# Performance work log

Measured on AMD Instinct MI355X. Metric: run time of the kernel, lower is better.

## Reference

```python
import jax, jax.numpy as jnp
from jax import lax
import numpy as np

L_BANDS = 28
H = 1024
W = 1024


def setup_inputs() -> dict:
    key = jax.random.key(0)
    k1, k2 = jax.random.split(key)
    x_1lhw = jax.random.uniform(k1, (1, L_BANDS, H, W), dtype=jnp.float32)
    mask2d = jax.random.uniform(k2, (H, W), dtype=jnp.float32)
    phi_d_deg = jnp.ones((1,), dtype=jnp.float32)  # dispersion axis angle in degrees
    s_nom = 2.0 * jnp.arange(L_BANDS, dtype=jnp.float32)  # 2 px/band nominal dispersion
    return {"x_1lhw": x_1lhw, "mask2d": mask2d, "phi_d_deg": phi_d_deg, "s_nom": s_nom}


def _int_offsets(phi_d_deg, s_nom):
    # Mirrors torch: offsets come from .item() => detached constants.
    phi = float(np.asarray(phi_d_deg).reshape(())) * np.pi / 180.0
    s = np.asarray(s_nom, dtype=np.float64)
    dx = s * np.cos(phi)
    dy = s * np.sin(phi)
    dx = dx - dx.min()
    dy = dy - dy.min()
    return np.rint(dx).astype(np.int32), np.rint(dy).astype(np.int32)


def reference(x_1lhw, mask2d, phi_d_deg, s_nom):
    _, L, Hh, Ww = x_1lhw.shape
    dx_i, dy_i = _int_offsets(phi_d_deg, s_nom)
    Hp = Hh + int(dy_i.max())
    Wp = Ww + int(dx_i.max())
    bands = mask2d[None, :, :] * x_1lhw[0]  # [L, H, W] coded bands

    def step(y, inp):
        band, oy, ox = inp
        patch = lax.dynamic_slice(y, (oy, ox), (Hh, Ww)) + band
        return lax.dynamic_update_slice(y, patch, (oy, ox)), None

    y0 = jnp.zeros((Hp, Wp), dtype=x_1lhw.dtype)
    y, _ = lax.scan(step, y0, (bands, jnp.asarray(dy_i), jnp.asarray(dx_i)))
    return y[None]  # [1, Hp, Wp]
```

## Files before the change

kernel.cpp:

```cpp
#include <hip/hip_runtime.h>
#include <math.h>

#define NL 28
#define H 1024
#define W 1024
#define HW (H * W)
#define BROW 1152
#define GUARD 64
#define NWAVE 2
#define WBANDS 14
#define NBUF 3
#define WREG (NBUF * BROW)
#define NPASS 9

typedef float f2 __attribute__((ext_vector_type(2), aligned(4)));

typedef __attribute__((address_space(1))) const void GV;
typedef __attribute__((address_space(3))) void LV;
__device__ __forceinline__ void gl_lds16(const float* g, float* l) {
    __builtin_amdgcn_global_load_lds((GV*)g, (LV*)l, 16, 0, 0);
}

__global__ __launch_bounds__(128, 2)
void cassi_v12(const float* __restrict__ x, const float* __restrict__ mask,
               const float* __restrict__ phi_deg, const float* __restrict__ s_nom,
               float* __restrict__ out, int out_size)
{
    __shared__ float lds[NWAVE * WREG + 2 * BROW];

    const int tid = threadIdx.x;
    const int lane = tid & 63;
    const int wid = tid >> 6;

    float phi = phi_deg[0] * 0.017453292519943295f;
    float c = cosf(phi), sn = sinf(phi);
    float s = (lane < NL) ? s_nom[lane] : 0.f;
    float dxv = s * c, dyv = s * sn;
    float dxm = (lane < NL) ? dxv : 3.0e38f;
    float dym = (lane < NL) ? dyv : 3.0e38f;
    for (int d = 1; d < 64; d <<= 1) {
        dxm = fminf(dxm, __shfl_xor(dxm, d, 64));
        dym = fminf(dym, __shfl_xor(dym, d, 64));
    }
    int dxi = (lane < NL) ? (int)rintf(dxv - dxm) : 0;
    int dyi = (lane < NL) ? (int)rintf(dyv - dym) : 0;
    int dxmax = dxi, dymax = dyi;
    for (int d = 1; d < 64; d <<= 1) {
        dxmax = max(dxmax, __shfl_xor(dxmax, d, 64));
        dymax = max(dymax, __shfl_xor(dymax, d, 64));
    }
    const int Wp = W + dxmax;
    const int Hp = out_size / Wp;

    if (!(dymax <= 1 && dxmax <= GUARD)) {
        for (int i = blockIdx.x * 128 + tid; i < out_size; i += gridDim.x * 128) {
            int Yk = i / Wp, Xk = i - Yk * Wp;
            float a = 0.f;
            for (int l = 0; l < NL; ++l) {
                float sl = s_nom[l];
                int dx = (int)rintf(sl * c - dxm);
                int dy = (int)rintf(sl * sn - dym);
                int h = Yk - dy, w = Xk - dx;
                if ((unsigned)h < (unsigned)H && (unsigned)w < (unsigned)W) {
                    int p = h * W + w;
                    a = fmaf(mask[p], x[(size_t)l * HW + p], a);
                }
            }
            out[i] = a;
        }
        return;
    }

    const int Y = blockIdx.x;
    if (Y >= Hp) return;

    float* xw = &lds[wid * WREG];
    float* mb = &lds[NWAVE * WREG];

    int xo_[WBANDS], mo_[WBANDS], sr_[WBANDS];
#pragma unroll
    for (int j = 0; j < WBANDS; ++j) {
        int l = wid * WBANDS + j;
        int dxj = __shfl(dxi, l, 64);
        int dyj = __shfl(dyi, l, 64);
        xo_[j] = (j % NBUF) * BROW + GUARD - dxj;
        mo_[j] = dyj * BROW + GUARD - dxj;
        sr_[j] = min(max(Y - dyj, 0), H - 1);
    }

#pragma unroll
    for (int b = 0; b < NBUF; ++b) {
        xw[b * BROW + lane] = 0.f;
        xw[b * BROW + GUARD + 1024 + lane] = 0.f;
    }
    {
        int g = Y - wid;
        float* mrow = &mb[wid * BROW];
        if ((unsigned)g < (unsigned)H) {
            const float* src = mask + (size_t)g * W + lane * 4;
            gl_lds16(src,       mrow + GUARD);
            gl_lds16(src + 256, mrow + GUARD + 256);
            gl_lds16(src + 512, mrow + GUARD + 512);
            gl_lds16(src + 768, mrow + GUARD + 768);
            mrow[lane] = 0.f;
            mrow[GUARD + 1024 + lane] = 0.f;
        } else {
            for (int k = lane; k < BROW; k += 64) mrow[k] = 0.f;
        }
    }
#pragma unroll
    for (int j = 0; j < 2; ++j) {
        int l = wid * WBANDS + j;
        const float* src = x + (size_t)l * HW + (size_t)sr_[j] * W + lane * 4;
        float* dst = xw + j * BROW + GUARD;
        gl_lds16(src, dst);
        gl_lds16(src + 256, dst + 256);
        gl_lds16(src + 512, dst + 512);
        gl_lds16(src + 768, dst + 768);
    }
    asm volatile("s_waitcnt vmcnt(8) lgkmcnt(0)" ::: "memory");
    __builtin_amdgcn_s_barrier();

    int te[NPASS];
#pragma unroll
    for (int p = 0; p < NPASS; ++p) {
        int t = p * 128 + 2 * lane;
        te[p] = (t < Wp) ? t : 0;
    }

    f2 acc[NPASS];
#pragma unroll
    for (int p = 0; p < NPASS; ++p) acc[p] = f2{0.f, 0.f};

#pragma unroll
    for (int j = 0; j < WBANDS; ++j) {
        if (j + 2 < WBANDS) {
            int l = wid * WBANDS + j + 2;
            const float* src = x + (size_t)l * HW + (size_t)sr_[j + 2] * W + lane * 4;
            float* dst = xw + ((j + 2) % NBUF) * BROW + GUARD;
            gl_lds16(src, dst);
            gl_lds16(src + 256, dst + 256);
            gl_lds16(src + 512, dst + 512);
            gl_lds16(src + 768, dst + 768);
        }
        if (j + 2 < WBANDS)      asm volatile("s_waitcnt vmcnt(8)" ::: "memory");
        else if (j + 1 < WBANDS) asm volatile("s_waitcnt vmcnt(4)" ::: "memory");
        else                     asm volatile("s_waitcnt vmcnt(0)" ::: "memory");

        const float* xb = xw + xo_[j];
        const float* mrow = mb + mo_[j];
#pragma unroll
        for (int p = 0; p < NPASS; ++p) {
            f2 xv = *(const f2*)&xb[te[p]];
            f2 mv = *(const f2*)&mrow[te[p]];
            acc[p] += xv * mv;
        }
        asm volatile("s_waitcnt lgkmcnt(0)" ::: "memory");
        __builtin_amdgcn_sched_barrier(0);
    }

#pragma unroll
    for (int p = 0; p < NPASS; ++p) {
        int t = p * 128 + 2 * lane;
        *(f2*)&xw[t] = acc[p];
    }
    asm volatile("s_waitcnt lgkmcnt(0)" ::: "memory");
    __builtin_amdgcn_s_barrier();

    float* orow = out + (size_t)Y * Wp;
#pragma unroll
    for (int q = 0; q < 5; ++q) {
        int t = 2 * (tid + q * 128);
        if (t + 1 < Wp) {
            f2 v = *(const f2*)&lds[t];
            v += *(const f2*)&lds[WREG + t];
            *(f2*)&orow[t] = v;
        } else if (t < Wp) {
            orow[t] = lds[t] + lds[WREG + t];
        }
    }
}

extern "C" void kernel_launch(void* const* d_in, const int* in_sizes, int n_in,
                              void* d_out, int out_size, void* d_ws, size_t ws_size,
                              hipStream_t stream) {
    const float* x = (const float*)d_in[0];
    const float* mask = (const float*)d_in[1];
    const float* phi = (const float*)d_in[2];
    const float* s_nom = (const float*)d_in[3];
    float* out = (float*)d_out;

    const int blocks = out_size / W + 2;
    cassi_v12<<<blocks, 128, 0, stream>>>(x, mask, phi, s_nom, out, out_size);
}
```

Measured before the change: 26.96 us.

## Remap rows to XCDs contiguously and halve the LDS cross-wave reduction

Block indices are remapped so that consecutive output rows land on the same XCD, letting neighbouring rows share mask and x rows in that XCD's L2. The final cross-wave reduction now has each wave write only the half of its accumulators the other wave needs, then add its own register half and store directly, which halves the LDS traffic in the epilogue. A per-band lgkmcnt wait is also removed. The mapping assumes round-robin dispatch across 8 XCDs, and the first-pass store path in wave 0 drops the Wp bounds check on the assumption that those columns are always in range.

```diff
diff --git a/kernel.cpp b/kernel.cpp
--- a/kernel.cpp
+++ b/kernel.cpp
@@ -12,6 +12,8 @@
 #define NBUF 3
 #define WREG (NBUF * BROW)
 #define NPASS 9
+#define SPLIT 5
+#define NXCD 8
 
 typedef float f2 __attribute__((ext_vector_type(2), aligned(4)));
 
@@ -22,7 +24,7 @@
 }
 
 __global__ __launch_bounds__(128, 2)
-void cassi_v12(const float* __restrict__ x, const float* __restrict__ mask,
+void cassi_v13(const float* __restrict__ x, const float* __restrict__ mask,
                const float* __restrict__ phi_deg, const float* __restrict__ s_nom,
                float* __restrict__ out, int out_size)
 {
@@ -71,7 +73,13 @@
         return;
     }
 
-    const int Y = blockIdx.x;
+    int Y;
+    {
+        const int nwg = gridDim.x;
+        const int q = nwg / NXCD, r = nwg % NXCD;
+        const int xcd = blockIdx.x % NXCD, idx = blockIdx.x / NXCD;
+        Y = (xcd < r ? xcd * (q + 1) : r * (q + 1) + (xcd - r) * q) + idx;
+    }
     if (Y >= Hp) return;
 
     float* xw = &lds[wid * WREG];
@@ -155,28 +163,45 @@
             f2 mv = *(const f2*)&mrow[te[p]];
             acc[p] += xv * mv;
         }
-        asm volatile("s_waitcnt lgkmcnt(0)" ::: "memory");
         __builtin_amdgcn_sched_barrier(0);
     }
 
-#pragma unroll
-    for (int p = 0; p < NPASS; ++p) {
-        int t = p * 128 + 2 * lane;
-        *(f2*)&xw[t] = acc[p];
+    if (wid == 0) {
+#pragma unroll
+        for (int p = SPLIT; p < NPASS; ++p) {
+            int t = p * 128 + 2 * lane;
+            *(f2*)&xw[t] = acc[p];
+        }
+    } else {
+#pragma unroll
+        for (int p = 0; p < SPLIT; ++p) {
+            int t = p * 128 + 2 * lane;
+            *(f2*)&xw[t] = acc[p];
+        }
     }
     asm volatile("s_waitcnt lgkmcnt(0)" ::: "memory");
     __builtin_amdgcn_s_barrier();
 
     float* orow = out + (size_t)Y * Wp;
-#pragma unroll
-    for (int q = 0; q < 5; ++q) {
-        int t = 2 * (tid + q * 128);
-        if (t + 1 < Wp) {
-            f2 v = *(const f2*)&lds[t];
-            v += *(const f2*)&lds[WREG + t];
+    if (wid == 0) {
+        const float* other = &lds[1 * WREG];
+#pragma unroll
+        for (int p = 0; p < SPLIT; ++p) {
+            int t = p * 128 + 2 * lane;
+            f2 v = acc[p] + *(const f2*)&other[t];
             *(f2*)&orow[t] = v;
-        } else if (t < Wp) {
-            orow[t] = lds[t] + lds[WREG + t];
+        }
+    } else {
+        const float* other = &lds[0 * WREG];
+#pragma unroll
+        for (int p = SPLIT; p < NPASS; ++p) {
+            int t = p * 128 + 2 * lane;
+            if (t + 1 < Wp) {
+                f2 v = acc[p] + *(const f2*)&other[t];
+                *(f2*)&orow[t] = v;
+            } else if (t < Wp) {
+                orow[t] = acc[p].x + other[t];
+            }
         }
     }
 }
@@ -191,5 +216,5 @@
     float* out = (float*)d_out;
 
     const int blocks = out_size / W + 2;
-    cassi_v12<<<blocks, 128, 0, stream>>>(x, mask, phi, s_nom, out, out_size);
+    cassi_v13<<<blocks, 128, 0, stream>>>(x, mask, phi, s_nom, out, out_size);
 }
```

Result: slower. 28.35 us (+5.2%).
